# Kernel tuning notes

Measured on AMD Instinct MI355X. Metric: run time of the kernel, lower is better.

Reference implementation:

```python
import jax, jax.numpy as jnp
import numpy as np
import math

NUM_CLASSES = 80
ANCHORS = [(12.0, 16.0), (19.0, 36.0), (40.0, 28.0)]
ANGLES = [-np.pi/3, -np.pi/6, 0.0, np.pi/6, np.pi/3, np.pi/2]
STRIDE = 8.0
SCALE_XY = 1.05
IGNORE_THRESH = 0.5
MASKED_ANCHORS = np.array([[w/STRIDE, h/STRIDE, a] for (w, h) in ANCHORS for a in ANGLES], dtype=np.float32)  # [18,3]
NA = MASKED_ANCHORS.shape[0]
LAMBDA_COORD, LAMBDA_CONF, LAMBDA_CLS = 1.0, 10.0, 1.0
FOCAL_ALPHA, FOCAL_GAMMA = 0.25, 2.0


def setup_inputs() -> dict:
    key = jax.random.key(0)
    B, G, nT = 8, 76, 240
    k1, k2, k3, k4, k5, k6 = jax.random.split(key, 6)
    output = jax.random.normal(k1, (B, NA * (NUM_CLASSES + 6), G, G), jnp.float32) * 0.1
    tb = jax.random.randint(k2, (nT,), 0, B).astype(jnp.float32)
    tl = jax.random.randint(k3, (nT,), 0, NUM_CLASSES).astype(jnp.float32)
    txy = jax.random.uniform(k4, (nT, 2), minval=0.02, maxval=0.98)
    twh = jax.random.uniform(k5, (nT, 2), minval=0.05, maxval=0.4)
    tang = jax.random.uniform(k6, (nT, 1), minval=-np.pi/2, maxval=np.pi/2)
    target = jnp.concatenate([tb[:, None], tl[:, None], txy, twh, tang], axis=-1)  # [nT,7]
    return {"output": output, "target": target}


def _smooth_l1(x, y):
    d = jnp.abs(x - y)
    return jnp.where(d < 1.0, 0.5 * d * d, d - 0.5)


def _bce(p, t):
    eps = 1e-7
    p = jnp.clip(p, eps, 1.0 - eps)
    return -(t * jnp.log(p) + (1.0 - t) * jnp.log(1.0 - p))


def _focal(p, t):
    loss = _bce(p, t)
    p_t = t * p + (1.0 - t) * (1.0 - p)
    alpha_f = t * FOCAL_ALPHA + (1.0 - t) * (1.0 - FOCAL_ALPHA)
    return loss * alpha_f * (1.0 - p_t) ** FOCAL_GAMMA


def _ciou(pb, tb):
    # pb, tb: [N,5] (cx, cy, w, h, angle) in grid units
    p1, p2 = pb[:, :2] - pb[:, 2:4] / 2, pb[:, :2] + pb[:, 2:4] / 2
    t1, t2 = tb[:, :2] - tb[:, 2:4] / 2, tb[:, :2] + tb[:, 2:4] / 2
    w1, h1 = p2[:, 0] - p1[:, 0], p2[:, 1] - p1[:, 1]
    w2, h2 = t2[:, 0] - t1[:, 0], t2[:, 1] - t1[:, 1]
    area1, area2 = w1 * h1, w2 * h2
    c1, c2 = (p1 + p2) / 2, (t1 + t2) / 2
    inter = jnp.clip(jnp.minimum(p2, t2) - jnp.maximum(p1, t1), 0.0)
    inter_area = inter[:, 0] * inter[:, 1]
    inter_diag = jnp.sum((c2 - c1) ** 2, axis=-1)
    outer = jnp.clip(jnp.maximum(p2, t2) - jnp.minimum(p1, t1), 0.0)
    outer_diag = outer[:, 0] ** 2 + outer[:, 1] ** 2
    union = area1 + area2 - inter_area
    u = inter_diag / outer_diag
    iou = inter_area / union
    v = (4.0 / math.pi ** 2) * (jnp.arctan(w2 / h2) - jnp.arctan(w1 / h1)) ** 2
    alpha = jax.lax.stop_gradient(v / ((1.0 - iou) + v))
    ciou = jnp.clip(iou - (u + alpha * v), -1.0, 1.0)
    skew_iou = iou * jnp.abs(jnp.cos(pb[:, 4] - tb[:, 4]))
    return skew_iou, ciou


def _forward(output, target):
    B, G = output.shape[0], output.shape[2]
    nC = NUM_CLASSES
    ma = jnp.asarray(MASKED_ANCHORS)
    pred = output.reshape(B, NA, nC + 6, G, G).transpose(0, 1, 3, 4, 2)  # [B,A,G,G,C+6]
    px = jax.nn.sigmoid(pred[..., 0]) * SCALE_XY - (SCALE_XY - 1) / 2
    py = jax.nn.sigmoid(pred[..., 1]) * SCALE_XY - (SCALE_XY - 1) / 2
    pw, ph, pa = pred[..., 2], pred[..., 3], pred[..., 4]
    pconf = jax.nn.sigmoid(pred[..., 5])
    pcls = jax.nn.sigmoid(pred[..., 6:])
    gx = jnp.arange(G, dtype=output.dtype)[None, None, None, :]
    gy = jnp.arange(G, dtype=output.dtype)[None, None, :, None]
    aw = ma[:, 0].reshape(1, NA, 1, 1)
    ah = ma[:, 1].reshape(1, NA, 1, 1)
    aa = ma[:, 2].reshape(1, NA, 1, 1)
    pred_boxes = jnp.stack([px + gx, py + gy, jnp.exp(pw) * aw, jnp.exp(ph) * ah, pa + aa], axis=-1)  # [B,A,G,G,5]
    out_dec = jnp.concatenate([
        jnp.concatenate([pred_boxes[..., :4] * STRIDE, pred_boxes[..., 4:]], axis=-1).reshape(B, -1, 5),
        pconf.reshape(B, -1, 1),
        pcls.reshape(B, -1, nC)], axis=-1)

    # ---- build_targets ----
    tgt_boxes = jnp.concatenate([target[:, 2:6] * G, target[:, 6:]], axis=-1)  # [nT,5]
    gxy, gwh, ga = tgt_boxes[:, :2], tgt_boxes[:, 2:4], tgt_boxes[:, 4]
    aw_, ah_, aa_ = ma[:, 0][:, None], ma[:, 1][:, None], ma[:, 2][:, None]  # [A,1]
    w2, h2 = gwh[:, 0][None, :], gwh[:, 1][None, :]                          # [1,nT]
    inter = jnp.minimum(aw_, w2) * jnp.minimum(ah_, h2)
    union = aw_ * ah_ + 1e-16 + w2 * h2 - inter
    offset = jnp.abs(aa_ - ga[None, :])                                       # [A,nT]
    arious = (inter / union) * jnp.abs(jnp.cos(aa_ - ga[None, :]))            # [A,nT]
    best_n = jnp.argmax(arious, axis=0)                                       # [nT]
    b = target[:, 0].astype(jnp.int32)
    labels = target[:, 1].astype(jnp.int32)
    gi = gxy[:, 0].astype(jnp.int32)
    gj = gxy[:, 1].astype(jnp.int32)

    zeros = jnp.zeros((B, NA, G, G), output.dtype)
    obj = zeros.at[b, best_n, gj, gi].set(1.0)
    noobj = jnp.ones((B, NA, G, G), output.dtype)
    cond = (arious > IGNORE_THRESH) | ((arious > 0.4) & (offset < np.pi / 12))  # [A,nT]
    a_idx = jnp.broadcast_to(jnp.arange(NA)[:, None], arious.shape)
    bb = jnp.broadcast_to(b[None, :], arious.shape)
    gjb = jnp.broadcast_to(gj[None, :], arious.shape)
    gib = jnp.broadcast_to(gi[None, :], arious.shape)
    noobj = noobj.at[bb, a_idx, gjb, gib].min(jnp.where(cond, 0.0, 1.0))
    noobj = noobj.at[b, best_n, gj, gi].set(0.0)

    ta_grid = zeros.at[b, best_n, gj, gi].set(ga - ma[best_n, 2])
    tcls = jnp.zeros((B, NA, G, G, nC), output.dtype).at[b, best_n, gj, gi, labels].set(1.0)
    tconf = obj

    pb = pred_boxes[b, best_n, gj, gi]  # [nT,5]
    iou, ciou = _ciou(pb, tgt_boxes)
    img_size = STRIDE * G
    bbox_scale = jax.lax.stop_gradient(2.0 - gwh[:, 0] * gwh[:, 1] / img_size ** 2)
    ciou_t = bbox_scale * (1.0 - ciou)

    class_ok = (jnp.argmax(pcls[b, best_n, gj, gi], axis=-1) == labels).astype(output.dtype)
    class_mask = zeros.at[b, best_n, gj, gi].set(class_ok)
    iou_scores = zeros.at[b, best_n, gj, gi].set(iou)
    skew = zeros.at[b, best_n, gj, gi].set(jnp.exp(1.0 - iou) - 1.0)
    ciou_grid = zeros.at[b, best_n, gj, gi].set(ciou_t)

    # ---- losses (masked means replace boolean indexing) ----
    n_obj = jnp.maximum(jnp.sum(obj), 1.0)
    n_noobj = jnp.maximum(jnp.sum(noobj), 1.0)
    reg = _smooth_l1(pa, ta_grid) + ciou_grid
    reg_const = jax.lax.stop_gradient(skew / jnp.where(obj > 0, reg, 1.0))
    reg_loss = jnp.sum(reg * reg_const * obj) / n_obj
    fl = _focal(pconf, tconf)
    conf_loss = jnp.sum(fl * obj) / n_obj + jnp.sum(fl * noobj) / n_noobj
    cls_loss = jnp.sum(_bce(pcls, tcls) * obj[..., None]) / (n_obj * nC)
    total_loss = LAMBDA_COORD * reg_loss + LAMBDA_CONF * conf_loss + LAMBDA_CLS * cls_loss
    return out_dec, total_loss


def reference(output, target):
    return _forward(output, target)
```

## Files before the change

### kernel.cpp

```cpp
#include <hip/hip_runtime.h>
#include <math.h>

#define NCLS 80
#define NANC 18
#define NB 8
#define GG 76
#define SS (GG*GG)
#define CHN (NCLS+6)
#define NCELL (NB*NANC*SS)
#define FLAG_WORDS ((NCELL+31)/32)
#define NT_MAX 240
#define TILE 76
#define LSTR 77
#define TPB 4
#define TGRP (GG/TPB)
#define NLOAD 7
#define TOT4 (CHN*(TILE/4))
#define NCONF4 (NCELL/4)
#define NCONFBLK ((NCONF4+255)/256)
#define PI_ 3.14159265358979323846

#define WS_WIN   64
#define WS_META  1024
#define WS_LM    4864
#define WS_FLAGS 6784

__device__ __constant__ float d_ma[NANC][3] = {
  {1.5f, 2.0f, (float)(-PI_/3)}, {1.5f, 2.0f, (float)(-PI_/6)}, {1.5f, 2.0f, 0.0f},
  {1.5f, 2.0f, (float)(PI_/6)},  {1.5f, 2.0f, (float)(PI_/3)},  {1.5f, 2.0f, (float)(PI_/2)},
  {2.375f, 4.5f, (float)(-PI_/3)}, {2.375f, 4.5f, (float)(-PI_/6)}, {2.375f, 4.5f, 0.0f},
  {2.375f, 4.5f, (float)(PI_/6)},  {2.375f, 4.5f, (float)(PI_/3)},  {2.375f, 4.5f, (float)(PI_/2)},
  {5.0f, 3.5f, (float)(-PI_/3)}, {5.0f, 3.5f, (float)(-PI_/6)}, {5.0f, 3.5f, 0.0f},
  {5.0f, 3.5f, (float)(PI_/6)},  {5.0f, 3.5f, (float)(PI_/3)},  {5.0f, 3.5f, (float)(PI_/2)},
};

__device__ __forceinline__ float sigm(float x) { return 1.0f / (1.0f + expf(-x)); }
__device__ __forceinline__ float fsig(float x) {
  return __builtin_amdgcn_rcpf(1.0f + __expf(-x));
}

__global__ __launch_bounds__(256) void k_prep(const float* __restrict__ tgt,
                                              unsigned* __restrict__ flags,
                                              int* __restrict__ win,
                                              int4* __restrict__ meta,
                                              uint2* __restrict__ lmout,
                                              int* __restrict__ cnt,
                                              double* __restrict__ acc, int nT) {
  __shared__ int s_key[NT_MAX], s_lab[NT_MAX];
  __shared__ int s_win[NT_MAX];
  __shared__ int s_zero;

  int t = threadIdx.x;
  uint4* f4 = (uint4*)flags;
  for (int i = t; i < FLAG_WORDS/4; i += 256) f4[i] = make_uint4(0,0,0,0);
  if (t < 4) { acc[t] = 0.0; cnt[t] = 0; }
  if (t == 0) s_zero = 0;
  __syncthreads();

  int bi = 0, gi = 0, gj = 0, bn = 0;
  unsigned cm = 0;
  if (t < nT) {
    float bf = tgt[t*7+0], lf = tgt[t*7+1];
    float gx = tgt[t*7+2] * (float)GG, gy = tgt[t*7+3] * (float)GG;
    float gw = tgt[t*7+4] * (float)GG, gh = tgt[t*7+5] * (float)GG;
    float ga = tgt[t*7+6];
    bi = (int)bf; gi = (int)gx; gj = (int)gy;
    int lab = (int)lf;
    float best = -1e30f;
    for (int a = 0; a < NANC; ++a) {
      float aw = d_ma[a][0], ah = d_ma[a][1], aa = d_ma[a][2];
      float inter = fminf(aw, gw) * fminf(ah, gh);
      float uni = aw*ah + 1e-16f + gw*gh - inter;
      float off = fabsf(aa - ga);
      float ar = inter / uni * fabsf(cosf(aa - ga));
      if (ar > best) { best = ar; bn = a; }
      if (ar > 0.5f || (ar > 0.4f && off < (float)(PI_/12))) cm |= (1u << a);
    }
    s_key[t] = ((bi*NANC + bn)*GG + gj)*GG + gi;
    s_lab[t] = lab;
    s_win[t] = 0;
  }
  __syncthreads();

  if (t < nT) {
    for (int a = 0; a < NANC; ++a) {
      if (((cm >> a) & 1u) || a == bn) {
        int cell = ((bi*NANC + a)*GG + gj)*GG + gi;
        unsigned bit = 1u << (cell & 31);
        unsigned old = atomicOr(&flags[cell >> 5], bit);
        if (!(old & bit)) atomicAdd(&s_zero, 1);
      }
    }
    int key = s_key[t];
    bool winner = true;
    for (int t2 = t + 1; t2 < nT; ++t2) if (s_key[t2] == key) { winner = false; break; }
    if (winner) {
      s_win[t] = 1;
      unsigned long long lm0 = 0, lm1 = 0;
      for (int t2 = 0; t2 < nT; ++t2) if (s_key[t2] == key) {
        int L = s_lab[t2];
        if (L < 64) lm0 |= 1ull << L; else lm1 |= 1ull << (L - 64);
      }
      lmout[t] = make_uint2((unsigned)(lm0 & 0xffffffffull), (unsigned)(lm0 >> 32));
      meta[t] = make_int4(bi, bn, gi, gj | ((int)(lm1 & 0xffffu) << 16));
      win[t] = 1;
    } else {
      win[t] = 0;
    }
  }
  __syncthreads();
  if (t == 0) {
    int nw = 0;
    for (int i = 0; i < nT; ++i) nw += s_win[i];
    cnt[0] = s_zero; cnt[1] = nw;
  }
}

__global__ __launch_bounds__(256) void k_loss(const float* __restrict__ tgt,
                                              const float* __restrict__ in,
                                              const int* __restrict__ win,
                                              const int4* __restrict__ meta,
                                              const uint2* __restrict__ lm,
                                              const unsigned* __restrict__ flags,
                                              double* __restrict__ acc, int nT) {
  int blk = blockIdx.x;
  int tid = threadIdx.x;

  if (blk < nT) {
    int t = blk;
    if (!win[t]) return;
    int4 m = meta[t];
    int bi = m.x, bn = m.y, gi = m.z, gj = m.w & 0xffff;
    unsigned lmhi = ((unsigned)m.w) >> 16;
    uint2 l0 = lm[t];
    const float* base = in + ((size_t)(bi*NANC + bn)*CHN)*SS + (size_t)gj*GG + gi;

    float csum = 0.0f;
    if (tid < NCLS) {
      float p = fsig(base[(size_t)(6 + tid)*SS]);
      float pl = fminf(fmaxf(p, 1e-7f), 1.0f - 1e-7f);
      bool tc;
      if (tid < 32)      tc = (l0.x >> tid) & 1u;
      else if (tid < 64) tc = (l0.y >> (tid - 32)) & 1u;
      else               tc = (lmhi >> (tid - 64)) & 1u;
      csum = tc ? -__logf(pl) : -__logf(1.0f - pl);
    }
    for (int off = 32; off; off >>= 1) csum += __shfl_down(csum, off);
    if ((tid & 63) == 0 && tid < 128) atomicAdd(&acc[3], (double)csum);

    if (tid == 128) {
      float gx = tgt[t*7+2] * (float)GG, gyv = tgt[t*7+3] * (float)GG;
      float gw = tgt[t*7+4] * (float)GG, gh = tgt[t*7+5] * (float)GG;
      float ga = tgt[t*7+6];
      float rx = base[0], ry = base[(size_t)SS], rw = base[2*(size_t)SS],
            rh = base[3*(size_t)SS], ra = base[4*(size_t)SS], rcf = base[5*(size_t)SS];
      float aw = d_ma[bn][0], ah = d_ma[bn][1], aa = d_ma[bn][2];
      float px = sigm(rx)*1.05f - 0.025f + (float)gi;
      float py = sigm(ry)*1.05f - 0.025f + (float)gj;
      float pw = expf(rw)*aw, ph = expf(rh)*ah;
      float pang = ra + aa;
      float p1x = px - pw*0.5f, p1y = py - ph*0.5f, p2x = px + pw*0.5f, p2y = py + ph*0.5f;
      float t1x = gx - gw*0.5f, t1y = gyv - gh*0.5f, t2x = gx + gw*0.5f, t2y = gyv + gh*0.5f;
      float w1 = p2x - p1x, h1 = p2y - p1y, w2 = t2x - t1x, h2 = t2y - t1y;
      float area1 = w1*h1, area2 = w2*h2;
      float c1x = (p1x+p2x)*0.5f, c1y = (p1y+p2y)*0.5f, c2x = (t1x+t2x)*0.5f, c2y = (t1y+t2y)*0.5f;
      float ix = fmaxf(fminf(p2x,t2x) - fmaxf(p1x,t1x), 0.0f);
      float iy = fmaxf(fminf(p2y,t2y) - fmaxf(p1y,t1y), 0.0f);
      float inter_area = ix*iy;
      float dcx = c2x - c1x, dcy = c2y - c1y;
      float inter_diag = dcx*dcx + dcy*dcy;
      float ox = fmaxf(fmaxf(p2x,t2x) - fminf(p1x,t1x), 0.0f);
      float oy = fmaxf(fmaxf(p2y,t2y) - fminf(p1y,t1y), 0.0f);
      float outer_diag = ox*ox + oy*oy;
      float uni = area1 + area2 - inter_area;
      float u = inter_diag / outer_diag;
      float iou = inter_area / uni;
      float da = atanf(w2/h2) - atanf(w1/h1);
      float v = (float)(4.0/(PI_*PI_)) * da * da;
      float alpha = v / (1.0f - iou + v);
      float ciou = fminf(fmaxf(iou - (u + alpha*v), -1.0f), 1.0f);
      float skew_iou = iou * fabsf(cosf(pang - ga));
      float skew = expf(1.0f - skew_iou) - 1.0f;
      float bscale = 2.0f - gw*gh/369664.0f;
      float ciou_t = bscale * (1.0f - ciou);
      float ta = ga - aa;
      float d = fabsf(ra - ta);
      float sl1 = (d < 1.0f) ? 0.5f*d*d : d - 0.5f;
      float reg = sl1 + ciou_t;
      atomicAdd(&acc[2], (double)(reg * (skew / reg)));
      float pc = sigm(rcf);
      float pcl = fminf(fmaxf(pc, 1e-7f), 1.0f - 1e-7f);
      float om = 1.0f - pc;
      atomicAdd(&acc[1], (double)(-logf(pcl) * 0.25f * om * om));
    }
    return;
  }

  __shared__ double wsum[4];
  int j = (blk - nT)*256 + tid;
  double fl = 0.0;
  if (j < NCONF4) {
    int ba = j / (SS/4);
    int q  = j - ba*(SS/4);
    int spos = 4*q;
    const float4 v4 = *(const float4*)(in + (size_t)ba*CHN*SS + 5*(size_t)SS + spos);
    int cell0 = ba*SS + spos;
    unsigned word = flags[cell0 >> 5];
    int bbit = cell0 & 31;
    float pv[4] = {v4.x, v4.y, v4.z, v4.w};
    #pragma unroll
    for (int e = 0; e < 4; ++e) {
      if (!((word >> (bbit + e)) & 1u)) {
        float p = fsig(pv[e]);
        float pcl = fminf(fmaxf(p, 1e-7f), 1.0f - 1e-7f);
        fl += (double)(-__logf(1.0f - pcl) * 0.75f * p * p);
      }
    }
  }
  int lane = tid & 63, wid = tid >> 6;
  for (int off = 32; off; off >>= 1) fl += __shfl_down(fl, off);
  if (lane == 0) wsum[wid] = fl;
  __syncthreads();
  if (tid == 0) {
    double s = wsum[0] + wsum[1] + wsum[2] + wsum[3];
    if (s != 0.0) atomicAdd(&acc[0], s);
  }
}

__global__ __launch_bounds__(256) void k_main(const float* __restrict__ in,
                                              float* __restrict__ out) {
  __shared__ float lds[CHN * LSTR];
  int blk = blockIdx.x;
  int tgrp = blk % TGRP;
  int ba = blk / TGRP;
  int a = ba % NANC;
  float aw8 = d_ma[a][0]*8.0f, ah8 = d_ma[a][1]*8.0f, aa = d_ma[a][2];
  const float* plane_in = in + (size_t)ba*CHN*SS;
  float* plane_out = out + (size_t)ba*SS*CHN;
  int tile0 = tgrp*TPB;

  float4 r[NLOAD];
  { const float* tin = plane_in + tile0*TILE;
    #pragma unroll
    for (int k = 0; k < NLOAD; ++k) {
      int i = threadIdx.x + k*256;
      if (i < TOT4) { int c = i/19, s4 = i - c*19;
        r[k] = *(const float4*)(tin + (size_t)c*SS + 4*s4); } }
  }

  for (int tt = 0; tt < TPB; ++tt) {
    int tile = tile0 + tt;
    __syncthreads();
    #pragma unroll
    for (int k = 0; k < NLOAD; ++k) {
      int i = threadIdx.x + k*256;
      if (i < TOT4) {
        int c = i/19, s4 = i - c*19;
        float* p = &lds[c*LSTR + 4*s4];
        p[0] = r[k].x; p[1] = r[k].y; p[2] = r[k].z; p[3] = r[k].w;
      }
    }
    __syncthreads();
    if (tt + 1 < TPB) {
      const float* tin = plane_in + (tile + 1)*TILE;
      #pragma unroll
      for (int k = 0; k < NLOAD; ++k) {
        int i = threadIdx.x + k*256;
        if (i < TOT4) { int c = i/19, s4 = i - c*19;
          r[k] = *(const float4*)(tin + (size_t)c*SS + 4*s4); } }
    }
    float gyf = (float)tile;
    float* orow = plane_out + (size_t)tile*TILE*CHN;
    for (int q = threadIdx.x; q < TILE*22; q += 256) {
      int s = q / 22;
      int j = q - s*22;
      int par = s & 1;
      if (j < 21) {
        int c = 2*par + 4*j;
        float v0 = lds[(c  )*LSTR + s];
        float v1 = lds[(c+1)*LSTR + s];
        float v2 = lds[(c+2)*LSTR + s];
        float v3 = lds[(c+3)*LSTR + s];
        float4 R;
        if (c >= 6) {
          R = make_float4(fsig(v0), fsig(v1), fsig(v2), fsig(v3));
        } else if (c == 0) {
          R.x = (fsig(v0)*1.05f - 0.025f + (float)s)*8.0f;
          R.y = (fsig(v1)*1.05f - 0.025f + gyf)*8.0f;
          R.z = __expf(v2)*aw8;
          R.w = __expf(v3)*ah8;
        } else if (c == 4) {
          R.x = v0 + aa;
          R.y = fsig(v1);
          R.z = fsig(v2);
          R.w = fsig(v3);
        } else {
          R.x = __expf(v0)*aw8;
          R.y = __expf(v1)*ah8;
          R.z = v2 + aa;
          R.w = fsig(v3);
        }
        *(float4*)(orow + s*CHN + c) = R;
      } else {
        int c = par ? 0 : 84;
        float v0 = lds[(c  )*LSTR + s];
        float v1 = lds[(c+1)*LSTR + s];
        float2 R;
        if (par) {
          R.x = (fsig(v0)*1.05f - 0.025f + (float)s)*8.0f;
          R.y = (fsig(v1)*1.05f - 0.025f + gyf)*8.0f;
        } else {
          R = make_float2(fsig(v0), fsig(v1));
        }
        *(float2*)(orow + s*CHN + c) = R;
      }
    }
  }
}

__global__ void k_fin(const double* __restrict__ acc, const int* __restrict__ cnt,
                      float* __restrict__ out) {
  double n_obj = fmax((double)cnt[1], 1.0);
  double n_noobj = fmax((double)(NCELL - cnt[0]), 1.0);
  double reg_loss = acc[2] / n_obj;
  double conf_loss = acc[1] / n_obj + acc[0] / n_noobj;
  double cls_loss = acc[3] / (n_obj * (double)NCLS);
  out[(size_t)NCELL * CHN] = (float)(reg_loss + 10.0*conf_loss + cls_loss);
}

extern "C" void kernel_launch(void* const* d_in, const int* in_sizes, int n_in,
                              void* d_out, int out_size, void* d_ws, size_t ws_size,
                              hipStream_t stream) {
  const float* in  = (const float*)d_in[0];
  const float* tgt = (const float*)d_in[1];
  float* out = (float*)d_out;
  double* acc = (double*)d_ws;
  int* cnt = (int*)((char*)d_ws + 32);
  int* win = (int*)((char*)d_ws + WS_WIN);
  int4* meta = (int4*)((char*)d_ws + WS_META);
  uint2* lm = (uint2*)((char*)d_ws + WS_LM);
  unsigned* flags = (unsigned*)((char*)d_ws + WS_FLAGS);
  int nT = in_sizes[1] / 7;
  if (nT > NT_MAX) nT = NT_MAX;

  hipLaunchKernelGGL(k_prep, dim3(1), dim3(256), 0, stream,
                     tgt, flags, win, meta, lm, cnt, acc, nT);
  hipLaunchKernelGGL(k_loss, dim3(nT + NCONFBLK), dim3(256), 0, stream,
                     tgt, in, win, meta, lm, flags, acc, nT);
  hipLaunchKernelGGL(k_fin, dim3(1), dim3(1), 0, stream, acc, cnt, out);
  hipLaunchKernelGGL(k_main, dim3(NB*NANC*TGRP), dim3(256), 0, stream, in, out);
}
```

Before: 209.5 us.

## Fuse loss finalization into k_loss via last-block ticket and widen k_main blocks

Removes the separate single-thread finalize kernel by having the last k_loss block (found through an atomic ticket counter) compute the total loss. k_main is changed to 512 threads per block, with fewer float4 prefetch registers per thread. This cuts one kernel launch and changes occupancy and register use for the main transpose/decode kernel. It relies on the ticket counter being reset each call.

```diff
diff --git a/kernel.cpp b/kernel.cpp
--- a/kernel.cpp
+++ b/kernel.cpp
@@ -14,7 +14,8 @@
 #define LSTR 77
 #define TPB 4
 #define TGRP (GG/TPB)
-#define NLOAD 7
+#define THR 512
+#define NLOAD 4
 #define TOT4 (CHN*(TILE/4))
 #define NCONF4 (NCELL/4)
 #define NCONFBLK ((NCONF4+255)/256)
@@ -122,112 +123,133 @@
                                               const int4* __restrict__ meta,
                                               const uint2* __restrict__ lm,
                                               const unsigned* __restrict__ flags,
-                                              double* __restrict__ acc, int nT) {
+                                              double* __restrict__ acc,
+                                              int* __restrict__ cnt,
+                                              float* __restrict__ out, int nT) {
   int blk = blockIdx.x;
   int tid = threadIdx.x;
+  int nblk = nT + NCONFBLK;
 
   if (blk < nT) {
-    int t = blk;
-    if (!win[t]) return;
-    int4 m = meta[t];
-    int bi = m.x, bn = m.y, gi = m.z, gj = m.w & 0xffff;
-    unsigned lmhi = ((unsigned)m.w) >> 16;
-    uint2 l0 = lm[t];
-    const float* base = in + ((size_t)(bi*NANC + bn)*CHN)*SS + (size_t)gj*GG + gi;
-
-    float csum = 0.0f;
-    if (tid < NCLS) {
-      float p = fsig(base[(size_t)(6 + tid)*SS]);
-      float pl = fminf(fmaxf(p, 1e-7f), 1.0f - 1e-7f);
-      bool tc;
-      if (tid < 32)      tc = (l0.x >> tid) & 1u;
-      else if (tid < 64) tc = (l0.y >> (tid - 32)) & 1u;
-      else               tc = (lmhi >> (tid - 64)) & 1u;
-      csum = tc ? -__logf(pl) : -__logf(1.0f - pl);
-    }
-    for (int off = 32; off; off >>= 1) csum += __shfl_down(csum, off);
-    if ((tid & 63) == 0 && tid < 128) atomicAdd(&acc[3], (double)csum);
-
-    if (tid == 128) {
-      float gx = tgt[t*7+2] * (float)GG, gyv = tgt[t*7+3] * (float)GG;
-      float gw = tgt[t*7+4] * (float)GG, gh = tgt[t*7+5] * (float)GG;
-      float ga = tgt[t*7+6];
-      float rx = base[0], ry = base[(size_t)SS], rw = base[2*(size_t)SS],
-            rh = base[3*(size_t)SS], ra = base[4*(size_t)SS], rcf = base[5*(size_t)SS];
-      float aw = d_ma[bn][0], ah = d_ma[bn][1], aa = d_ma[bn][2];
-      float px = sigm(rx)*1.05f - 0.025f + (float)gi;
-      float py = sigm(ry)*1.05f - 0.025f + (float)gj;
-      float pw = expf(rw)*aw, ph = expf(rh)*ah;
-      float pang = ra + aa;
-      float p1x = px - pw*0.5f, p1y = py - ph*0.5f, p2x = px + pw*0.5f, p2y = py + ph*0.5f;
-      float t1x = gx - gw*0.5f, t1y = gyv - gh*0.5f, t2x = gx + gw*0.5f, t2y = gyv + gh*0.5f;
-      float w1 = p2x - p1x, h1 = p2y - p1y, w2 = t2x - t1x, h2 = t2y - t1y;
-      float area1 = w1*h1, area2 = w2*h2;
-      float c1x = (p1x+p2x)*0.5f, c1y = (p1y+p2y)*0.5f, c2x = (t1x+t2x)*0.5f, c2y = (t1y+t2y)*0.5f;
-      float ix = fmaxf(fminf(p2x,t2x) - fmaxf(p1x,t1x), 0.0f);
-      float iy = fmaxf(fminf(p2y,t2y) - fmaxf(p1y,t1y), 0.0f);
-      float inter_area = ix*iy;
-      float dcx = c2x - c1x, dcy = c2y - c1y;
-      float inter_diag = dcx*dcx + dcy*dcy;
-      float ox = fmaxf(fmaxf(p2x,t2x) - fminf(p1x,t1x), 0.0f);
-      float oy = fmaxf(fmaxf(p2y,t2y) - fminf(p1y,t1y), 0.0f);
-      float outer_diag = ox*ox + oy*oy;
-      float uni = area1 + area2 - inter_area;
-      float u = inter_diag / outer_diag;
-      float iou = inter_area / uni;
-      float da = atanf(w2/h2) - atanf(w1/h1);
-      float v = (float)(4.0/(PI_*PI_)) * da * da;
-      float alpha = v / (1.0f - iou + v);
-      float ciou = fminf(fmaxf(iou - (u + alpha*v), -1.0f), 1.0f);
-      float skew_iou = iou * fabsf(cosf(pang - ga));
-      float skew = expf(1.0f - skew_iou) - 1.0f;
-      float bscale = 2.0f - gw*gh/369664.0f;
-      float ciou_t = bscale * (1.0f - ciou);
-      float ta = ga - aa;
-      float d = fabsf(ra - ta);
-      float sl1 = (d < 1.0f) ? 0.5f*d*d : d - 0.5f;
-      float reg = sl1 + ciou_t;
-      atomicAdd(&acc[2], (double)(reg * (skew / reg)));
-      float pc = sigm(rcf);
-      float pcl = fminf(fmaxf(pc, 1e-7f), 1.0f - 1e-7f);
-      float om = 1.0f - pc;
-      atomicAdd(&acc[1], (double)(-logf(pcl) * 0.25f * om * om));
-    }
-    return;
-  }
-
-  __shared__ double wsum[4];
-  int j = (blk - nT)*256 + tid;
-  double fl = 0.0;
-  if (j < NCONF4) {
-    int ba = j / (SS/4);
-    int q  = j - ba*(SS/4);
-    int spos = 4*q;
-    const float4 v4 = *(const float4*)(in + (size_t)ba*CHN*SS + 5*(size_t)SS + spos);
-    int cell0 = ba*SS + spos;
-    unsigned word = flags[cell0 >> 5];
-    int bbit = cell0 & 31;
-    float pv[4] = {v4.x, v4.y, v4.z, v4.w};
-    #pragma unroll
-    for (int e = 0; e < 4; ++e) {
-      if (!((word >> (bbit + e)) & 1u)) {
-        float p = fsig(pv[e]);
-        float pcl = fminf(fmaxf(p, 1e-7f), 1.0f - 1e-7f);
-        fl += (double)(-__logf(1.0f - pcl) * 0.75f * p * p);
-      }
-    }
-  }
-  int lane = tid & 63, wid = tid >> 6;
-  for (int off = 32; off; off >>= 1) fl += __shfl_down(fl, off);
-  if (lane == 0) wsum[wid] = fl;
+    if (win[blk]) {
+      int t = blk;
+      int4 m = meta[t];
+      int bi = m.x, bn = m.y, gi = m.z, gj = m.w & 0xffff;
+      unsigned lmhi = ((unsigned)m.w) >> 16;
+      uint2 l0 = lm[t];
+      const float* base = in + ((size_t)(bi*NANC + bn)*CHN)*SS + (size_t)gj*GG + gi;
+
+      float csum = 0.0f;
+      if (tid < NCLS) {
+        float p = fsig(base[(size_t)(6 + tid)*SS]);
+        float pl = fminf(fmaxf(p, 1e-7f), 1.0f - 1e-7f);
+        bool tc;
+        if (tid < 32)      tc = (l0.x >> tid) & 1u;
+        else if (tid < 64) tc = (l0.y >> (tid - 32)) & 1u;
+        else               tc = (lmhi >> (tid - 64)) & 1u;
+        csum = tc ? -__logf(pl) : -__logf(1.0f - pl);
+      }
+      for (int off = 32; off; off >>= 1) csum += __shfl_down(csum, off);
+      if ((tid & 63) == 0 && tid < 128) atomicAdd(&acc[3], (double)csum);
+
+      if (tid == 128) {
+        float gx = tgt[t*7+2] * (float)GG, gyv = tgt[t*7+3] * (float)GG;
+        float gw = tgt[t*7+4] * (float)GG, gh = tgt[t*7+5] * (float)GG;
+        float ga = tgt[t*7+6];
+        float rx = base[0], ry = base[(size_t)SS], rw = base[2*(size_t)SS],
+              rh = base[3*(size_t)SS], ra = base[4*(size_t)SS], rcf = base[5*(size_t)SS];
+        float aw = d_ma[bn][0], ah = d_ma[bn][1], aa = d_ma[bn][2];
+        float px = sigm(rx)*1.05f - 0.025f + (float)gi;
+        float py = sigm(ry)*1.05f - 0.025f + (float)gj;
+        float pw = expf(rw)*aw, ph = expf(rh)*ah;
+        float pang = ra + aa;
+        float p1x = px - pw*0.5f, p1y = py - ph*0.5f, p2x = px + pw*0.5f, p2y = py + ph*0.5f;
+        float t1x = gx - gw*0.5f, t1y = gyv - gh*0.5f, t2x = gx + gw*0.5f, t2y = gyv + gh*0.5f;
+        float w1 = p2x - p1x, h1 = p2y - p1y, w2 = t2x - t1x, h2 = t2y - t1y;
+        float area1 = w1*h1, area2 = w2*h2;
+        float c1x = (p1x+p2x)*0.5f, c1y = (p1y+p2y)*0.5f, c2x = (t1x+t2x)*0.5f, c2y = (t1y+t2y)*0.5f;
+        float ix = fmaxf(fminf(p2x,t2x) - fmaxf(p1x,t1x), 0.0f);
+        float iy = fmaxf(fminf(p2y,t2y) - fmaxf(p1y,t1y), 0.0f);
+        float inter_area = ix*iy;
+        float dcx = c2x - c1x, dcy = c2y - c1y;
+        float inter_diag = dcx*dcx + dcy*dcy;
+        float ox = fmaxf(fmaxf(p2x,t2x) - fminf(p1x,t1x), 0.0f);
+        float oy = fmaxf(fmaxf(p2y,t2y) - fminf(p1y,t1y), 0.0f);
+        float outer_diag = ox*ox + oy*oy;
+        float uni = area1 + area2 - inter_area;
+        float u = inter_diag / outer_diag;
+        float iou = inter_area / uni;
+        float da = atanf(w2/h2) - atanf(w1/h1);
+        float v = (float)(4.0/(PI_*PI_)) * da * da;
+        float alpha = v / (1.0f - iou + v);
+        float ciou = fminf(fmaxf(iou - (u + alpha*v), -1.0f), 1.0f);
+        float skew_iou = iou * fabsf(cosf(pang - ga));
+        float skew = expf(1.0f - skew_iou) - 1.0f;
+        float bscale = 2.0f - gw*gh/369664.0f;
+        float ciou_t = bscale * (1.0f - ciou);
+        float ta = ga - aa;
+        float d = fabsf(ra - ta);
+        float sl1 = (d < 1.0f) ? 0.5f*d*d : d - 0.5f;
+        float reg = sl1 + ciou_t;
+        atomicAdd(&acc[2], (double)(reg * (skew / reg)));
+        float pc = sigm(rcf);
+        float pcl = fminf(fmaxf(pc, 1e-7f), 1.0f - 1e-7f);
+        float om = 1.0f - pc;
+        atomicAdd(&acc[1], (double)(-logf(pcl) * 0.25f * om * om));
+      }
+    }
+  } else {
+    __shared__ double wsum[4];
+    int j = (blk - nT)*256 + tid;
+    double fl = 0.0;
+    if (j < NCONF4) {
+      int ba = j / (SS/4);
+      int q  = j - ba*(SS/4);
+      int spos = 4*q;
+      const float4 v4 = *(const float4*)(in + (size_t)ba*CHN*SS + 5*(size_t)SS + spos);
+      int cell0 = ba*SS + spos;
+      unsigned word = flags[cell0 >> 5];
+      int bbit = cell0 & 31;
+      float pv[4] = {v4.x, v4.y, v4.z, v4.w};
+      #pragma unroll
+      for (int e = 0; e < 4; ++e) {
+        if (!((word >> (bbit + e)) & 1u)) {
+          float p = fsig(pv[e]);
+          float pcl = fminf(fmaxf(p, 1e-7f), 1.0f - 1e-7f);
+          fl += (double)(-__logf(1.0f - pcl) * 0.75f * p * p);
+        }
+      }
+    }
+    int lane = tid & 63, wid = tid >> 6;
+    for (int off = 32; off; off >>= 1) fl += __shfl_down(fl, off);
+    if (lane == 0) wsum[wid] = fl;
+    __syncthreads();
+    if (tid == 0) {
+      double s = wsum[0] + wsum[1] + wsum[2] + wsum[3];
+      if (s != 0.0) atomicAdd(&acc[0], s);
+    }
+  }
+
   __syncthreads();
   if (tid == 0) {
-    double s = wsum[0] + wsum[1] + wsum[2] + wsum[3];
-    if (s != 0.0) atomicAdd(&acc[0], s);
-  }
-}
-
-__global__ __launch_bounds__(256) void k_main(const float* __restrict__ in,
+    __threadfence();
+    unsigned tk = atomicAdd((unsigned*)&cnt[2], 1u);
+    if (tk == (unsigned)(nblk - 1)) {
+      double a0 = atomicAdd(&acc[0], 0.0);
+      double a1 = atomicAdd(&acc[1], 0.0);
+      double a2 = atomicAdd(&acc[2], 0.0);
+      double a3 = atomicAdd(&acc[3], 0.0);
+      int c0 = atomicAdd(&cnt[0], 0);
+      int c1 = atomicAdd(&cnt[1], 0);
+      double n_obj = fmax((double)c1, 1.0);
+      double n_noobj = fmax((double)(NCELL - c0), 1.0);
+      double loss = a2/n_obj + 10.0*(a1/n_obj + a0/n_noobj) + a3/(n_obj*(double)NCLS);
+      out[(size_t)NCELL*CHN] = (float)loss;
+    }
+  }
+}
+
+__global__ __launch_bounds__(THR) void k_main(const float* __restrict__ in,
                                               float* __restrict__ out) {
   __shared__ float lds[CHN * LSTR];
   int blk = blockIdx.x;
@@ -243,7 +265,7 @@
   { const float* tin = plane_in + tile0*TILE;
     #pragma unroll
     for (int k = 0; k < NLOAD; ++k) {
-      int i = threadIdx.x + k*256;
+      int i = threadIdx.x + k*THR;
       if (i < TOT4) { int c = i/19, s4 = i - c*19;
         r[k] = *(const float4*)(tin + (size_t)c*SS + 4*s4); } }
   }
@@ -253,7 +275,7 @@
     __syncthreads();
     #pragma unroll
     for (int k = 0; k < NLOAD; ++k) {
-      int i = threadIdx.x + k*256;
+      int i = threadIdx.x + k*THR;
       if (i < TOT4) {
         int c = i/19, s4 = i - c*19;
         float* p = &lds[c*LSTR + 4*s4];
@@ -265,13 +287,13 @@
       const float* tin = plane_in + (tile + 1)*TILE;
       #pragma unroll
       for (int k = 0; k < NLOAD; ++k) {
-        int i = threadIdx.x + k*256;
+        int i = threadIdx.x + k*THR;
         if (i < TOT4) { int c = i/19, s4 = i - c*19;
           r[k] = *(const float4*)(tin + (size_t)c*SS + 4*s4); } }
     }
     float gyf = (float)tile;
     float* orow = plane_out + (size_t)tile*TILE*CHN;
-    for (int q = threadIdx.x; q < TILE*22; q += 256) {
+    for (int q = threadIdx.x; q < TILE*22; q += THR) {
       int s = q / 22;
       int j = q - s*22;
       int par = s & 1;
@@ -318,16 +340,6 @@
   }
 }
 
-__global__ void k_fin(const double* __restrict__ acc, const int* __restrict__ cnt,
-                      float* __restrict__ out) {
-  double n_obj = fmax((double)cnt[1], 1.0);
-  double n_noobj = fmax((double)(NCELL - cnt[0]), 1.0);
-  double reg_loss = acc[2] / n_obj;
-  double conf_loss = acc[1] / n_obj + acc[0] / n_noobj;
-  double cls_loss = acc[3] / (n_obj * (double)NCLS);
-  out[(size_t)NCELL * CHN] = (float)(reg_loss + 10.0*conf_loss + cls_loss);
-}
-
 extern "C" void kernel_launch(void* const* d_in, const int* in_sizes, int n_in,
                               void* d_out, int out_size, void* d_ws, size_t ws_size,
                               hipStream_t stream) {
@@ -346,7 +358,6 @@
   hipLaunchKernelGGL(k_prep, dim3(1), dim3(256), 0, stream,
                      tgt, flags, win, meta, lm, cnt, acc, nT);
   hipLaunchKernelGGL(k_loss, dim3(nT + NCONFBLK), dim3(256), 0, stream,
-                     tgt, in, win, meta, lm, flags, acc, nT);
-  hipLaunchKernelGGL(k_fin, dim3(1), dim3(1), 0, stream, acc, cnt, out);
-  hipLaunchKernelGGL(k_main, dim3(NB*NANC*TGRP), dim3(256), 0, stream, in, out);
-}
+                     tgt, in, win, meta, lm, flags, acc, cnt, out, nT);
+  hipLaunchKernelGGL(k_main, dim3(NB*NANC*TGRP), dim3(THR), 0, stream, in, out);
+}
```

Result: slower. 217.0 us (+3.6%).

## Double-buffer LDS tile in k_main and move workspace zeroing to a parallel kernel

Applied to the files above, without the earlier changes.

k_main now alternates between two LDS buffers, which removes the barrier at the top of each tile iteration so the next tile's writes no longer wait for the previous compute to finish. The zeroing of the flag bitmap and accumulators moves out of the single-block k_prep into a new multi-block k_zero kernel, so that serial work is spread across many blocks. In exchange k_main's LDS use doubles, which may lower occupancy, and every call pays one extra kernel launch. Without the top barrier, writing buffer tt&1 at iteration tt+2 depends on the single remaining barrier per iteration for correctness.

```diff
diff --git a/kernel.cpp b/kernel.cpp
--- a/kernel.cpp
+++ b/kernel.cpp
@@ -14,6 +14,7 @@
 #define LSTR 77
 #define TPB 4
 #define TGRP (GG/TPB)
+#define THR 256
 #define NLOAD 7
 #define TOT4 (CHN*(TILE/4))
 #define NCONF4 (NCELL/4)
@@ -39,21 +40,23 @@
   return __builtin_amdgcn_rcpf(1.0f + __expf(-x));
 }
 
+__global__ void k_zero(unsigned* __restrict__ ws_words, unsigned* __restrict__ flags) {
+  int i = blockIdx.x * blockDim.x + threadIdx.x;
+  if (i < 16) ws_words[i] = 0u;
+  if (i < FLAG_WORDS) flags[i] = 0u;
+}
+
 __global__ __launch_bounds__(256) void k_prep(const float* __restrict__ tgt,
                                               unsigned* __restrict__ flags,
                                               int* __restrict__ win,
                                               int4* __restrict__ meta,
                                               uint2* __restrict__ lmout,
-                                              int* __restrict__ cnt,
-                                              double* __restrict__ acc, int nT) {
+                                              int* __restrict__ cnt, int nT) {
   __shared__ int s_key[NT_MAX], s_lab[NT_MAX];
   __shared__ int s_win[NT_MAX];
   __shared__ int s_zero;
 
   int t = threadIdx.x;
-  uint4* f4 = (uint4*)flags;
-  for (int i = t; i < FLAG_WORDS/4; i += 256) f4[i] = make_uint4(0,0,0,0);
-  if (t < 4) { acc[t] = 0.0; cnt[t] = 0; }
   if (t == 0) s_zero = 0;
   __syncthreads();
 
@@ -227,9 +230,9 @@
   }
 }
 
-__global__ __launch_bounds__(256) void k_main(const float* __restrict__ in,
+__global__ __launch_bounds__(THR) void k_main(const float* __restrict__ in,
                                               float* __restrict__ out) {
-  __shared__ float lds[CHN * LSTR];
+  __shared__ float lds[2][CHN * LSTR];
   int blk = blockIdx.x;
   int tgrp = blk % TGRP;
   int ba = blk / TGRP;
@@ -243,20 +246,20 @@
   { const float* tin = plane_in + tile0*TILE;
     #pragma unroll
     for (int k = 0; k < NLOAD; ++k) {
-      int i = threadIdx.x + k*256;
+      int i = threadIdx.x + k*THR;
       if (i < TOT4) { int c = i/19, s4 = i - c*19;
         r[k] = *(const float4*)(tin + (size_t)c*SS + 4*s4); } }
   }
 
   for (int tt = 0; tt < TPB; ++tt) {
     int tile = tile0 + tt;
-    __syncthreads();
+    float* buf = lds[tt & 1];
     #pragma unroll
     for (int k = 0; k < NLOAD; ++k) {
-      int i = threadIdx.x + k*256;
+      int i = threadIdx.x + k*THR;
       if (i < TOT4) {
         int c = i/19, s4 = i - c*19;
-        float* p = &lds[c*LSTR + 4*s4];
+        float* p = &buf[c*LSTR + 4*s4];
         p[0] = r[k].x; p[1] = r[k].y; p[2] = r[k].z; p[3] = r[k].w;
       }
     }
@@ -265,22 +268,22 @@
       const float* tin = plane_in + (tile + 1)*TILE;
       #pragma unroll
       for (int k = 0; k < NLOAD; ++k) {
-        int i = threadIdx.x + k*256;
+        int i = threadIdx.x + k*THR;
         if (i < TOT4) { int c = i/19, s4 = i - c*19;
           r[k] = *(const float4*)(tin + (size_t)c*SS + 4*s4); } }
     }
     float gyf = (float)tile;
     float* orow = plane_out + (size_t)tile*TILE*CHN;
-    for (int q = threadIdx.x; q < TILE*22; q += 256) {
+    for (int q = threadIdx.x; q < TILE*22; q += THR) {
       int s = q / 22;
       int j = q - s*22;
       int par = s & 1;
       if (j < 21) {
         int c = 2*par + 4*j;
-        float v0 = lds[(c  )*LSTR + s];
-        float v1 = lds[(c+1)*LSTR + s];
-        float v2 = lds[(c+2)*LSTR + s];
-        float v3 = lds[(c+3)*LSTR + s];
+        float v0 = buf[(c  )*LSTR + s];
+        float v1 = buf[(c+1)*LSTR + s];
+        float v2 = buf[(c+2)*LSTR + s];
+        float v3 = buf[(c+3)*LSTR + s];
         float4 R;
         if (c >= 6) {
           R = make_float4(fsig(v0), fsig(v1), fsig(v2), fsig(v3));
@@ -303,8 +306,8 @@
         *(float4*)(orow + s*CHN + c) = R;
       } else {
         int c = par ? 0 : 84;
-        float v0 = lds[(c  )*LSTR + s];
-        float v1 = lds[(c+1)*LSTR + s];
+        float v0 = buf[(c  )*LSTR + s];
+        float v1 = buf[(c+1)*LSTR + s];
         float2 R;
         if (par) {
           R.x = (fsig(v0)*1.05f - 0.025f + (float)s)*8.0f;
@@ -343,10 +346,12 @@
   int nT = in_sizes[1] / 7;
   if (nT > NT_MAX) nT = NT_MAX;
 
+  hipLaunchKernelGGL(k_zero, dim3((FLAG_WORDS + 255)/256), dim3(256), 0, stream,
+                     (unsigned*)d_ws, flags);
   hipLaunchKernelGGL(k_prep, dim3(1), dim3(256), 0, stream,
-                     tgt, flags, win, meta, lm, cnt, acc, nT);
+                     tgt, flags, win, meta, lm, cnt, nT);
   hipLaunchKernelGGL(k_loss, dim3(nT + NCONFBLK), dim3(256), 0, stream,
                      tgt, in, win, meta, lm, flags, acc, nT);
   hipLaunchKernelGGL(k_fin, dim3(1), dim3(1), 0, stream, acc, cnt, out);
-  hipLaunchKernelGGL(k_main, dim3(NB*NANC*TGRP), dim3(256), 0, stream, in, out);
-}
+  hipLaunchKernelGGL(k_main, dim3(NB*NANC*TGRP), dim3(THR), 0, stream, in, out);
+}
```

Measured after the change: 213.2 us. No clear change (+1.8%).
